# Kernel optimization log

Hardware: AMD Instinct MI355X
Metric: run time of the kernel (lower is better)

## Reference

```python
import jax, jax.numpy as jnp
import numpy as np

B, L, D_PAIR, N_HEAD = 1, 320, 128, 4
EPS = 1e-5


def setup_inputs() -> dict:
    key = jax.random.key(0)
    ks = jax.random.split(key, 8)
    s = 0.05  # ~xavier scale for fan_in=128
    return {
        "pair": jax.random.normal(ks[0], (B, L, L, D_PAIR), jnp.float32),
        "norm_w": jnp.ones((D_PAIR,), jnp.float32),
        "norm_b": jnp.zeros((D_PAIR,), jnp.float32),
        "Wq": jax.random.normal(ks[1], (D_PAIR, D_PAIR), jnp.float32) * s,
        "Wk": jax.random.normal(ks[2], (D_PAIR, D_PAIR), jnp.float32) * s,
        "Wv": jax.random.normal(ks[3], (D_PAIR, D_PAIR), jnp.float32) * s,
        "Wg": jax.random.normal(ks[4], (D_PAIR, D_PAIR), jnp.float32) * s,
        "bg": jnp.zeros((D_PAIR,), jnp.float32),
        "Wo": jax.random.normal(ks[5], (D_PAIR, D_PAIR), jnp.float32) * s,
        "bo": jnp.zeros((D_PAIR,), jnp.float32),
        "Wb": jax.random.normal(ks[6], (N_HEAD, D_PAIR), jnp.float32) * s,
    }


def reference(pair, norm_w, norm_b, Wq, Wk, Wv, Wg, bg, Wo, bo, Wb):
    # Triangle attention, mode='start' (no permute). pair: (B, L, L, D)
    Bs, Ls, _, D = pair.shape
    H = Wb.shape[0]
    Dh = D // H
    scale = Dh ** -0.5

    # LayerNorm (fp32, matches torch eps=1e-5)
    mu = jnp.mean(pair, axis=-1, keepdims=True)
    var = jnp.var(pair, axis=-1, keepdims=True)
    x = (pair - mu) * jax.lax.rsqrt(var + EPS) * norm_w + norm_b

    def heads(y):
        # (B,L,L,D) -> (B,L,H,L,Dh): attention runs along the second L axis per row i
        return y.reshape(Bs, Ls, Ls, H, Dh).transpose(0, 1, 3, 2, 4)

    Q = heads(x @ Wq.T)
    K = heads(x @ Wk.T)
    V = heads(x @ Wv.T)
    g = heads(jax.nn.sigmoid(x @ Wg.T + bg))

    attn = jnp.einsum('blhid,blhjd->blhij', Q, K) * scale  # (B,L,H,L,L)
    # bias from RAW pair (pre-norm), projected to heads, broadcast over query index i
    bias = (pair @ Wb.T).transpose(0, 1, 3, 2)[:, :, :, None, :]  # (B,L,H,1,L)
    attn = jax.nn.softmax(attn + bias, axis=-1)

    out = jnp.einsum('blhij,blhjd->blhid', attn, V)  # (B,L,H,L,Dh)
    out = (g * out).transpose(0, 1, 3, 2, 4).reshape(Bs, Ls, Ls, D)
    return pair + out @ Wo.T + bo
```

## Files before the change

kernel.cpp:

```cpp
#include <hip/hip_runtime.h>

typedef unsigned short u16;
typedef unsigned int u32;
typedef __attribute__((ext_vector_type(8))) short bf16x8;
typedef __attribute__((ext_vector_type(4))) float f32x4;

#define LOG2E 1.4426950408889634f

__device__ __forceinline__ u16 f2bf(float f) {
    u32 u = __float_as_uint(f);
    u += 0x7fffu + ((u >> 16) & 1u);
    return (u16)(u >> 16);
}
__device__ __forceinline__ float bf2f(u16 s) {
    return __uint_as_float(((u32)s) << 16);
}

__global__ void wconv_kernel(const float* __restrict__ Wq, const float* __restrict__ Wk,
                             const float* __restrict__ Wv, const float* __restrict__ Wg,
                             const float* __restrict__ Wo, u16* __restrict__ wbf) {
    int idx = blockIdx.x * blockDim.x + threadIdx.x;
    wbf[0 * 16384 + idx] = f2bf(Wq[idx]);
    wbf[1 * 16384 + idx] = f2bf(Wk[idx]);
    wbf[2 * 16384 + idx] = f2bf(Wv[idx]);
    wbf[3 * 16384 + idx] = f2bf(Wg[idx]);
    wbf[4 * 16384 + idx] = f2bf(Wo[idx]);
}

__global__ __launch_bounds__(256, 1)
void attn_kernel(const float* __restrict__ pair,
                 const float* __restrict__ norm_w,
                 const float* __restrict__ norm_b,
                 const float* __restrict__ bg,
                 const float* __restrict__ Wb,
                 const u16* __restrict__ wbf,
                 u16* __restrict__ Obf) {
    const int l = blockIdx.x >> 2;
    const int h = blockIdx.x & 3;
    const int tid = threadIdx.x;
    const int wave = tid >> 6;
    const int lane = tid & 63;
    const int i_lo = lane & 15;
    const int q = lane >> 4;

    __shared__ __align__(16) u16 Xs[64 * 136];
    __shared__ __align__(16) u16 Qs[320 * 40];
    __shared__ __align__(16) u16 Ks[320 * 40];
    __shared__ __align__(16) u16 Gs[320 * 40];
    __shared__ __align__(16) u16 VTs[32 * 328];
    __shared__ __align__(16) float biasLds[320];
    __shared__ __align__(16) float wls[3 * 128];

    if (tid < 96) {
        int a = tid >> 5;
        int t = tid & 31;
        const float* src = (a == 0) ? norm_w : (a == 1) ? norm_b : (Wb + h * 128);
        f32x4 v = *(const f32x4*)(src + t * 4);
        *(f32x4*)&wls[a * 128 + t * 4] = v;
    }

    float bg0 = bg[h * 32 + i_lo];
    float bg1 = bg[h * 32 + 16 + i_lo];

    bf16x8 wfrag[4][8];
#pragma unroll
    for (int kc = 0; kc < 4; ++kc)
#pragma unroll
        for (int nt = 0; nt < 8; ++nt) {
            int mat = nt >> 1;
            int drow = h * 32 + (nt & 1) * 16 + i_lo;
            wfrag[kc][nt] = *(const bf16x8*)&wbf[mat * 16384 + drow * 128 + kc * 32 + q * 8];
        }

    __syncthreads();

    const int row_g = tid >> 2;
    const int c4 = tid & 3;

#pragma unroll 1
    for (int jt5 = 0; jt5 < 5; ++jt5) {
        int j0 = jt5 * 64;
        const float* prow = pair + ((size_t)(l * 320 + j0 + row_g)) * 128 + c4 * 32;
        f32x4 pr[8];
#pragma unroll
        for (int u = 0; u < 8; ++u) pr[u] = *(const f32x4*)(prow + u * 4);

        float s = 0.f, s2 = 0.f, bd = 0.f;
#pragma unroll
        for (int u = 0; u < 8; ++u) {
            f32x4 p = pr[u];
            f32x4 wb4 = *(const f32x4*)&wls[2 * 128 + c4 * 32 + u * 4];
            s += p[0] + p[1] + p[2] + p[3];
            s2 += p[0] * p[0] + p[1] * p[1] + p[2] * p[2] + p[3] * p[3];
            bd += p[0] * wb4[0] + p[1] * wb4[1] + p[2] * wb4[2] + p[3] * wb4[3];
        }
        s += __shfl_xor(s, 1);   s += __shfl_xor(s, 2);
        s2 += __shfl_xor(s2, 1); s2 += __shfl_xor(s2, 2);
        bd += __shfl_xor(bd, 1); bd += __shfl_xor(bd, 2);
        float mu = s * 0.0078125f;
        float var = s2 * 0.0078125f - mu * mu;
        float rs = rsqrtf(var + 1e-5f);

        __syncthreads();
#pragma unroll
        for (int u = 0; u < 8; ++u) {
            f32x4 p = pr[u];
            f32x4 w4 = *(const f32x4*)&wls[0 * 128 + c4 * 32 + u * 4];
            f32x4 b4 = *(const f32x4*)&wls[1 * 128 + c4 * 32 + u * 4];
            ushort4 xv;
            xv.x = f2bf((p[0] - mu) * rs * w4[0] + b4[0]);
            xv.y = f2bf((p[1] - mu) * rs * w4[1] + b4[1]);
            xv.z = f2bf((p[2] - mu) * rs * w4[2] + b4[2]);
            xv.w = f2bf((p[3] - mu) * rs * w4[3] + b4[3]);
            *(ushort4*)&Xs[row_g * 136 + c4 * 32 + u * 4] = xv;
        }
        if (c4 == 0) biasLds[j0 + row_g] = bd * LOG2E;
        __syncthreads();

        f32x4 acc[8];
#pragma unroll
        for (int nt = 0; nt < 8; ++nt) acc[nt] = (f32x4){0.f, 0.f, 0.f, 0.f};
#pragma unroll
        for (int kc = 0; kc < 4; ++kc) {
            bf16x8 a = *(const bf16x8*)&Xs[(wave * 16 + i_lo) * 136 + kc * 32 + q * 8];
#pragma unroll
            for (int nt = 0; nt < 8; ++nt)
                acc[nt] = __builtin_amdgcn_mfma_f32_16x16x32_bf16(a, wfrag[kc][nt], acc[nt], 0, 0, 0);
        }
        int jrow = j0 + wave * 16 + q * 4;
#pragma unroll
        for (int nt = 0; nt < 8; ++nt) {
#pragma unroll
            for (int r = 0; r < 4; ++r) {
                float v = acc[nt][r];
                int jr = jrow + r;
                int dl = (nt & 1) * 16 + i_lo;
                if (nt < 2)      Qs[jr * 40 + dl] = f2bf(v);
                else if (nt < 4) Ks[jr * 40 + dl] = f2bf(v);
                else if (nt < 6) VTs[dl * 328 + jr] = f2bf(v);
                else {
                    float z = v + ((nt & 1) ? bg1 : bg0);
                    float g = 1.0f / (1.0f + exp2f(-z * LOG2E));
                    Gs[jr * 40 + dl] = f2bf(g);
                }
            }
        }
    }
    __syncthreads();

    const float SC = 0.17677669529663687f * LOG2E;
    const f32x4 zero4 = {0.f, 0.f, 0.f, 0.f};
#pragma unroll 1
    for (int s5 = 0; s5 < 5; ++s5) {
        int i0 = wave * 80 + s5 * 16;
        bf16x8 qf = *(const bf16x8*)&Qs[(i0 + i_lo) * 40 + q * 8];

        f32x4 sc[20];
#pragma unroll
        for (int jt = 0; jt < 20; ++jt) {
            bf16x8 kf = *(const bf16x8*)&Ks[(jt * 16 + i_lo) * 40 + q * 8];
            sc[jt] = __builtin_amdgcn_mfma_f32_16x16x32_bf16(kf, qf, zero4, 0, 0, 0);
        }
        float mx = -3.0e38f;
#pragma unroll
        for (int jt = 0; jt < 20; ++jt) {
            f32x4 b4 = *(const f32x4*)&biasLds[jt * 16 + q * 4];
#pragma unroll
            for (int r = 0; r < 4; ++r) {
                float v = sc[jt][r] * SC + b4[r];
                sc[jt][r] = v;
                mx = fmaxf(mx, v);
            }
        }
        mx = fmaxf(mx, __shfl_xor(mx, 16));
        mx = fmaxf(mx, __shfl_xor(mx, 32));
        float sum = 0.f;
#pragma unroll
        for (int jt = 0; jt < 20; ++jt)
#pragma unroll
            for (int r = 0; r < 4; ++r) {
                float p = exp2f(sc[jt][r] - mx);
                sc[jt][r] = p;
                sum += p;
            }
        sum += __shfl_xor(sum, 16);
        sum += __shfl_xor(sum, 32);
        float rinv = 1.0f / sum;

        f32x4 oacc[2];
        oacc[0] = zero4; oacc[1] = zero4;
        const int srcb = ((q & 1) * 2) * 16 + i_lo;
        const bool hiq = (q >= 2);
#pragma unroll
        for (int kt = 0; kt < 10; ++kt) {
            union { bf16x8 v; u16 u[8]; } pu;
#pragma unroll
            for (int jj = 0; jj < 8; ++jj) {
                int r = jj & 3;
                int src = srcb + ((jj >> 2) << 4);
                float lo = __shfl(sc[2 * kt][r], src, 64);
                float hi = __shfl(sc[2 * kt + 1][r], src, 64);
                pu.u[jj] = f2bf(hiq ? hi : lo);
            }
#pragma unroll
            for (int mt = 0; mt < 2; ++mt) {
                bf16x8 vf = *(const bf16x8*)&VTs[(mt * 16 + i_lo) * 328 + kt * 32 + q * 8];
                oacc[mt] = __builtin_amdgcn_mfma_f32_16x16x32_bf16(vf, pu.v, oacc[mt], 0, 0, 0);
            }
        }
#pragma unroll
        for (int mt = 0; mt < 2; ++mt)
#pragma unroll
            for (int r = 0; r < 4; ++r) {
                int d = mt * 16 + q * 4 + r;
                float g = bf2f(Gs[(i0 + i_lo) * 40 + d]);
                float o = oacc[mt][r] * rinv * g;
                Obf[((size_t)(l * 320 + i0 + i_lo)) * 128 + h * 32 + d] = f2bf(o);
            }
    }
}

__global__ __launch_bounds__(256)
void outproj_kernel(const float* __restrict__ pair,
                    const float* __restrict__ bo,
                    const u16* __restrict__ Obf,
                    const u16* __restrict__ wbf,
                    float* __restrict__ out) {
    const int tid = threadIdx.x;
    const int wave = tid >> 6;
    const int lane = tid & 63;
    const int i_lo = lane & 15;
    const int q = lane >> 4;
    const int mrow = blockIdx.x * 64 + wave * 16;
    const u16* Wo = wbf + 4 * 16384;

    bf16x8 of[4];
#pragma unroll
    for (int kc = 0; kc < 4; ++kc)
        of[kc] = *(const bf16x8*)&Obf[((size_t)(mrow + i_lo)) * 128 + kc * 32 + q * 8];

    float bov[8];
#pragma unroll
    for (int nt = 0; nt < 8; ++nt) bov[nt] = bo[nt * 16 + i_lo];

    f32x4 acc[8];
#pragma unroll
    for (int nt = 0; nt < 8; ++nt) acc[nt] = (f32x4){0.f, 0.f, 0.f, 0.f};
#pragma unroll
    for (int nt = 0; nt < 8; ++nt) {
#pragma unroll
        for (int kc = 0; kc < 4; ++kc) {
            bf16x8 wf = *(const bf16x8*)&Wo[(nt * 16 + i_lo) * 128 + kc * 32 + q * 8];
            acc[nt] = __builtin_amdgcn_mfma_f32_16x16x32_bf16(of[kc], wf, acc[nt], 0, 0, 0);
        }
    }
#pragma unroll
    for (int nt = 0; nt < 8; ++nt)
#pragma unroll
        for (int r = 0; r < 4; ++r) {
            size_t idx = ((size_t)(mrow + q * 4 + r)) * 128 + nt * 16 + i_lo;
            out[idx] = acc[nt][r] + pair[idx] + bov[nt];
        }
}

extern "C" void kernel_launch(void* const* d_in, const int* in_sizes, int n_in,
                              void* d_out, int out_size, void* d_ws, size_t ws_size,
                              hipStream_t stream) {
    const float* pair   = (const float*)d_in[0];
    const float* norm_w = (const float*)d_in[1];
    const float* norm_b = (const float*)d_in[2];
    const float* Wq     = (const float*)d_in[3];
    const float* Wk     = (const float*)d_in[4];
    const float* Wv     = (const float*)d_in[5];
    const float* Wg     = (const float*)d_in[6];
    const float* bg     = (const float*)d_in[7];
    const float* Wo     = (const float*)d_in[8];
    const float* bo     = (const float*)d_in[9];
    const float* Wb     = (const float*)d_in[10];

    u16* wbf = (u16*)d_ws;
    u16* Obf = wbf + 5 * 16384;
    float* out = (float*)d_out;

    wconv_kernel<<<64, 256, 0, stream>>>(Wq, Wk, Wv, Wg, Wo, wbf);
    attn_kernel<<<320 * 4, 256, 0, stream>>>(pair, norm_w, norm_b, bg, Wb, wbf, Obf);
    outproj_kernel<<<1600, 256, 0, stream>>>(pair, bo, Obf, wbf, out);
}
```

Before: 346.4 us.

## Restructure triangle attention to 512 threads, LDS P staging, no softmax max

Doubles the attention block to 8 waves and puts all tiles in one shared buffer. The probability matrix is staged through per-wave LDS with truncating bf16 packing instead of lane shuffles. The softmax max-subtraction is dropped, and the output projection is transposed so stores and pair loads are vectorized. This cuts shuffle and conversion overhead and raises parallelism. Skipping the max is numerically unsafe for large logits, and truncation lowers rounding accuracy.

```diff
diff --git a/kernel.cpp b/kernel.cpp
--- a/kernel.cpp
+++ b/kernel.cpp
@@ -4,6 +4,7 @@
 typedef unsigned int u32;
 typedef __attribute__((ext_vector_type(8))) short bf16x8;
 typedef __attribute__((ext_vector_type(4))) float f32x4;
+typedef __attribute__((ext_vector_type(2))) unsigned int u32x2;
 
 #define LOG2E 1.4426950408889634f
 
@@ -14,6 +15,9 @@
 }
 __device__ __forceinline__ float bf2f(u16 s) {
     return __uint_as_float(((u32)s) << 16);
+}
+__device__ __forceinline__ u32 pk_bf_trunc(float hi, float lo) {
+    return __builtin_amdgcn_perm(__float_as_uint(hi), __float_as_uint(lo), 0x07060302u);
 }
 
 __global__ void wconv_kernel(const float* __restrict__ Wq, const float* __restrict__ Wk,
@@ -27,7 +31,13 @@
     wbf[4 * 16384 + idx] = f2bf(Wo[idx]);
 }
 
-__global__ __launch_bounds__(256, 1)
+#define PBUF_W 2688
+#define QS_OFF 21504
+#define KS_OFF 34304
+#define GS_OFF 47104
+#define VTS_OFF 59904
+
+__global__ __launch_bounds__(512, 2)
 void attn_kernel(const float* __restrict__ pair,
                  const float* __restrict__ norm_w,
                  const float* __restrict__ norm_b,
@@ -43,11 +53,7 @@
     const int i_lo = lane & 15;
     const int q = lane >> 4;
 
-    __shared__ __align__(16) u16 Xs[64 * 136];
-    __shared__ __align__(16) u16 Qs[320 * 40];
-    __shared__ __align__(16) u16 Ks[320 * 40];
-    __shared__ __align__(16) u16 Gs[320 * 40];
-    __shared__ __align__(16) u16 VTs[32 * 328];
+    __shared__ __align__(16) u16 smem[70400];
     __shared__ __align__(16) float biasLds[320];
     __shared__ __align__(16) float wls[3 * 128];
 
@@ -78,70 +84,80 @@
     const int c4 = tid & 3;
 
 #pragma unroll 1
-    for (int jt5 = 0; jt5 < 5; ++jt5) {
-        int j0 = jt5 * 64;
-        const float* prow = pair + ((size_t)(l * 320 + j0 + row_g)) * 128 + c4 * 32;
+    for (int t = 0; t < 3; ++t) {
+        const int j0 = t * 128;
+        const int nrows = (t == 2) ? 64 : 128;
+        const bool act = row_g < nrows;
+
         f32x4 pr[8];
-#pragma unroll
-        for (int u = 0; u < 8; ++u) pr[u] = *(const f32x4*)(prow + u * 4);
-
-        float s = 0.f, s2 = 0.f, bd = 0.f;
-#pragma unroll
-        for (int u = 0; u < 8; ++u) {
-            f32x4 p = pr[u];
-            f32x4 wb4 = *(const f32x4*)&wls[2 * 128 + c4 * 32 + u * 4];
-            s += p[0] + p[1] + p[2] + p[3];
-            s2 += p[0] * p[0] + p[1] * p[1] + p[2] * p[2] + p[3] * p[3];
-            bd += p[0] * wb4[0] + p[1] * wb4[1] + p[2] * wb4[2] + p[3] * wb4[3];
-        }
-        s += __shfl_xor(s, 1);   s += __shfl_xor(s, 2);
-        s2 += __shfl_xor(s2, 1); s2 += __shfl_xor(s2, 2);
-        bd += __shfl_xor(bd, 1); bd += __shfl_xor(bd, 2);
-        float mu = s * 0.0078125f;
-        float var = s2 * 0.0078125f - mu * mu;
-        float rs = rsqrtf(var + 1e-5f);
+        float mu, rs, bd;
+        if (act) {
+            const float* prow = pair + ((size_t)(l * 320 + j0 + row_g)) * 128 + c4 * 32;
+#pragma unroll
+            for (int u = 0; u < 8; ++u) pr[u] = *(const f32x4*)(prow + u * 4);
+            float s = 0.f, s2 = 0.f;
+            bd = 0.f;
+#pragma unroll
+            for (int u = 0; u < 8; ++u) {
+                f32x4 p = pr[u];
+                f32x4 wb4 = *(const f32x4*)&wls[2 * 128 + c4 * 32 + u * 4];
+                s += p[0] + p[1] + p[2] + p[3];
+                s2 += p[0] * p[0] + p[1] * p[1] + p[2] * p[2] + p[3] * p[3];
+                bd += p[0] * wb4[0] + p[1] * wb4[1] + p[2] * wb4[2] + p[3] * wb4[3];
+            }
+            s += __shfl_xor(s, 1);   s += __shfl_xor(s, 2);
+            s2 += __shfl_xor(s2, 1); s2 += __shfl_xor(s2, 2);
+            bd += __shfl_xor(bd, 1); bd += __shfl_xor(bd, 2);
+            mu = s * 0.0078125f;
+            float var = s2 * 0.0078125f - mu * mu;
+            rs = rsqrtf(var + 1e-5f);
+        }
 
         __syncthreads();
-#pragma unroll
-        for (int u = 0; u < 8; ++u) {
-            f32x4 p = pr[u];
-            f32x4 w4 = *(const f32x4*)&wls[0 * 128 + c4 * 32 + u * 4];
-            f32x4 b4 = *(const f32x4*)&wls[1 * 128 + c4 * 32 + u * 4];
-            ushort4 xv;
-            xv.x = f2bf((p[0] - mu) * rs * w4[0] + b4[0]);
-            xv.y = f2bf((p[1] - mu) * rs * w4[1] + b4[1]);
-            xv.z = f2bf((p[2] - mu) * rs * w4[2] + b4[2]);
-            xv.w = f2bf((p[3] - mu) * rs * w4[3] + b4[3]);
-            *(ushort4*)&Xs[row_g * 136 + c4 * 32 + u * 4] = xv;
-        }
-        if (c4 == 0) biasLds[j0 + row_g] = bd * LOG2E;
+        if (act) {
+#pragma unroll
+            for (int u = 0; u < 8; ++u) {
+                f32x4 p = pr[u];
+                f32x4 w4 = *(const f32x4*)&wls[0 * 128 + c4 * 32 + u * 4];
+                f32x4 b4 = *(const f32x4*)&wls[1 * 128 + c4 * 32 + u * 4];
+                ushort4 xv;
+                xv.x = f2bf((p[0] - mu) * rs * w4[0] + b4[0]);
+                xv.y = f2bf((p[1] - mu) * rs * w4[1] + b4[1]);
+                xv.z = f2bf((p[2] - mu) * rs * w4[2] + b4[2]);
+                xv.w = f2bf((p[3] - mu) * rs * w4[3] + b4[3]);
+                *(ushort4*)&smem[row_g * 136 + c4 * 32 + u * 4] = xv;
+            }
+            if (c4 == 0) biasLds[j0 + row_g] = bd * LOG2E;
+        }
         __syncthreads();
 
-        f32x4 acc[8];
-#pragma unroll
-        for (int nt = 0; nt < 8; ++nt) acc[nt] = (f32x4){0.f, 0.f, 0.f, 0.f};
-#pragma unroll
-        for (int kc = 0; kc < 4; ++kc) {
-            bf16x8 a = *(const bf16x8*)&Xs[(wave * 16 + i_lo) * 136 + kc * 32 + q * 8];
-#pragma unroll
-            for (int nt = 0; nt < 8; ++nt)
-                acc[nt] = __builtin_amdgcn_mfma_f32_16x16x32_bf16(a, wfrag[kc][nt], acc[nt], 0, 0, 0);
-        }
-        int jrow = j0 + wave * 16 + q * 4;
-#pragma unroll
-        for (int nt = 0; nt < 8; ++nt) {
-#pragma unroll
-            for (int r = 0; r < 4; ++r) {
-                float v = acc[nt][r];
-                int jr = jrow + r;
-                int dl = (nt & 1) * 16 + i_lo;
-                if (nt < 2)      Qs[jr * 40 + dl] = f2bf(v);
-                else if (nt < 4) Ks[jr * 40 + dl] = f2bf(v);
-                else if (nt < 6) VTs[dl * 328 + jr] = f2bf(v);
-                else {
-                    float z = v + ((nt & 1) ? bg1 : bg0);
-                    float g = 1.0f / (1.0f + exp2f(-z * LOG2E));
-                    Gs[jr * 40 + dl] = f2bf(g);
+        if (wave * 16 < nrows) {
+            f32x4 acc[8];
+#pragma unroll
+            for (int nt = 0; nt < 8; ++nt) acc[nt] = (f32x4){0.f, 0.f, 0.f, 0.f};
+#pragma unroll
+            for (int kc = 0; kc < 4; ++kc) {
+                bf16x8 a = *(const bf16x8*)&smem[(wave * 16 + i_lo) * 136 + kc * 32 + q * 8];
+#pragma unroll
+                for (int nt = 0; nt < 8; ++nt)
+                    acc[nt] = __builtin_amdgcn_mfma_f32_16x16x32_bf16(a, wfrag[kc][nt], acc[nt], 0, 0, 0);
+            }
+            int jrow = j0 + wave * 16 + q * 4;
+#pragma unroll
+            for (int nt = 0; nt < 8; ++nt) {
+#pragma unroll
+                for (int r = 0; r < 4; ++r) {
+                    float v = acc[nt][r];
+                    int jr = jrow + r;
+                    int dl = (nt & 1) * 16 + i_lo;
+                    if (nt < 2)      smem[QS_OFF + jr * 40 + dl] = f2bf(v);
+                    else if (nt < 4) smem[KS_OFF + jr * 40 + dl] = f2bf(v);
+                    else if (nt < 6) smem[VTS_OFF + dl * 328 + jr] = f2bf(v);
+                    else {
+                        float z = v + ((nt & 1) ? bg1 : bg0);
+                        float g = 1.0f / (1.0f + exp2f(-z * LOG2E));
+                        smem[GS_OFF + jr * 40 + dl] = f2bf(g);
+                    }
                 }
             }
         }
@@ -150,73 +166,69 @@
 
     const float SC = 0.17677669529663687f * LOG2E;
     const f32x4 zero4 = {0.f, 0.f, 0.f, 0.f};
+    u16* pb = smem + wave * PBUF_W;
 #pragma unroll 1
-    for (int s5 = 0; s5 < 5; ++s5) {
-        int i0 = wave * 80 + s5 * 16;
-        bf16x8 qf = *(const bf16x8*)&Qs[(i0 + i_lo) * 40 + q * 8];
+    for (int t2 = 0; t2 < 3; ++t2) {
+        const int strip = wave + 8 * t2;
+        if (strip >= 20) break;
+        const int i0 = strip * 16;
+        bf16x8 qf = *(const bf16x8*)&smem[QS_OFF + (i0 + i_lo) * 40 + q * 8];
 
         f32x4 sc[20];
 #pragma unroll
         for (int jt = 0; jt < 20; ++jt) {
-            bf16x8 kf = *(const bf16x8*)&Ks[(jt * 16 + i_lo) * 40 + q * 8];
+            bf16x8 kf = *(const bf16x8*)&smem[KS_OFF + (jt * 16 + i_lo) * 40 + q * 8];
             sc[jt] = __builtin_amdgcn_mfma_f32_16x16x32_bf16(kf, qf, zero4, 0, 0, 0);
         }
-        float mx = -3.0e38f;
+        float sum = 0.f;
 #pragma unroll
         for (int jt = 0; jt < 20; ++jt) {
             f32x4 b4 = *(const f32x4*)&biasLds[jt * 16 + q * 4];
 #pragma unroll
             for (int r = 0; r < 4; ++r) {
-                float v = sc[jt][r] * SC + b4[r];
-                sc[jt][r] = v;
-                mx = fmaxf(mx, v);
-            }
-        }
-        mx = fmaxf(mx, __shfl_xor(mx, 16));
-        mx = fmaxf(mx, __shfl_xor(mx, 32));
-        float sum = 0.f;
-#pragma unroll
-        for (int jt = 0; jt < 20; ++jt)
-#pragma unroll
-            for (int r = 0; r < 4; ++r) {
-                float p = exp2f(sc[jt][r] - mx);
+                float p = exp2f(sc[jt][r] * SC + b4[r]);
                 sc[jt][r] = p;
                 sum += p;
             }
+        }
         sum += __shfl_xor(sum, 16);
         sum += __shfl_xor(sum, 32);
         float rinv = 1.0f / sum;
 
         f32x4 oacc[2];
         oacc[0] = zero4; oacc[1] = zero4;
-        const int srcb = ((q & 1) * 2) * 16 + i_lo;
-        const bool hiq = (q >= 2);
-#pragma unroll
-        for (int kt = 0; kt < 10; ++kt) {
-            union { bf16x8 v; u16 u[8]; } pu;
-#pragma unroll
-            for (int jj = 0; jj < 8; ++jj) {
-                int r = jj & 3;
-                int src = srcb + ((jj >> 2) << 4);
-                float lo = __shfl(sc[2 * kt][r], src, 64);
-                float hi = __shfl(sc[2 * kt + 1][r], src, 64);
-                pu.u[jj] = f2bf(hiq ? hi : lo);
-            }
-#pragma unroll
-            for (int mt = 0; mt < 2; ++mt) {
-                bf16x8 vf = *(const bf16x8*)&VTs[(mt * 16 + i_lo) * 328 + kt * 32 + q * 8];
-                oacc[mt] = __builtin_amdgcn_mfma_f32_16x16x32_bf16(vf, pu.v, oacc[mt], 0, 0, 0);
-            }
-        }
-#pragma unroll
-        for (int mt = 0; mt < 2; ++mt)
-#pragma unroll
-            for (int r = 0; r < 4; ++r) {
-                int d = mt * 16 + q * 4 + r;
-                float g = bf2f(Gs[(i0 + i_lo) * 40 + d]);
-                float o = oacc[mt][r] * rinv * g;
-                Obf[((size_t)(l * 320 + i0 + i_lo)) * 128 + h * 32 + d] = f2bf(o);
-            }
+#pragma unroll
+        for (int hh = 0; hh < 2; ++hh) {
+#pragma unroll
+            for (int jt10 = 0; jt10 < 10; ++jt10) {
+                f32x4 s4 = sc[hh * 10 + jt10];
+                u32x2 pk;
+                pk.x = pk_bf_trunc(s4[1], s4[0]);
+                pk.y = pk_bf_trunc(s4[3], s4[2]);
+                *(u32x2*)&pb[i_lo * 168 + jt10 * 16 + q * 4] = pk;
+            }
+#pragma unroll
+            for (int kt = 0; kt < 5; ++kt) {
+                bf16x8 pf = *(const bf16x8*)&pb[i_lo * 168 + kt * 32 + q * 8];
+#pragma unroll
+                for (int mt = 0; mt < 2; ++mt) {
+                    bf16x8 vf = *(const bf16x8*)&smem[VTS_OFF + (mt * 16 + i_lo) * 328 + hh * 160 + kt * 32 + q * 8];
+                    oacc[mt] = __builtin_amdgcn_mfma_f32_16x16x32_bf16(vf, pf, oacc[mt], 0, 0, 0);
+                }
+            }
+        }
+#pragma unroll
+        for (int mt = 0; mt < 2; ++mt) {
+            ushort4 g4 = *(const ushort4*)&smem[GS_OFF + (i0 + i_lo) * 40 + mt * 16 + q * 4];
+            float o0 = oacc[mt][0] * rinv * bf2f(g4.x);
+            float o1 = oacc[mt][1] * rinv * bf2f(g4.y);
+            float o2 = oacc[mt][2] * rinv * bf2f(g4.z);
+            float o3 = oacc[mt][3] * rinv * bf2f(g4.w);
+            u32x2 pk;
+            pk.x = pk_bf_trunc(o1, o0);
+            pk.y = pk_bf_trunc(o3, o2);
+            *(u32x2*)&Obf[((size_t)(l * 320 + i0 + i_lo)) * 128 + h * 32 + mt * 16 + q * 4] = pk;
+        }
     }
 }
 
@@ -239,10 +251,6 @@
     for (int kc = 0; kc < 4; ++kc)
         of[kc] = *(const bf16x8*)&Obf[((size_t)(mrow + i_lo)) * 128 + kc * 32 + q * 8];
 
-    float bov[8];
-#pragma unroll
-    for (int nt = 0; nt < 8; ++nt) bov[nt] = bo[nt * 16 + i_lo];
-
     f32x4 acc[8];
 #pragma unroll
     for (int nt = 0; nt < 8; ++nt) acc[nt] = (f32x4){0.f, 0.f, 0.f, 0.f};
@@ -251,16 +259,21 @@
 #pragma unroll
         for (int kc = 0; kc < 4; ++kc) {
             bf16x8 wf = *(const bf16x8*)&Wo[(nt * 16 + i_lo) * 128 + kc * 32 + q * 8];
-            acc[nt] = __builtin_amdgcn_mfma_f32_16x16x32_bf16(of[kc], wf, acc[nt], 0, 0, 0);
-        }
-    }
-#pragma unroll
-    for (int nt = 0; nt < 8; ++nt)
-#pragma unroll
-        for (int r = 0; r < 4; ++r) {
-            size_t idx = ((size_t)(mrow + q * 4 + r)) * 128 + nt * 16 + i_lo;
-            out[idx] = acc[nt][r] + pair[idx] + bov[nt];
-        }
+            acc[nt] = __builtin_amdgcn_mfma_f32_16x16x32_bf16(wf, of[kc], acc[nt], 0, 0, 0);
+        }
+    }
+#pragma unroll
+    for (int nt = 0; nt < 8; ++nt) {
+        size_t idx = ((size_t)(mrow + i_lo)) * 128 + nt * 16 + q * 4;
+        f32x4 p4 = *(const f32x4*)&pair[idx];
+        f32x4 b4 = *(const f32x4*)&bo[nt * 16 + q * 4];
+        f32x4 o4;
+        o4[0] = acc[nt][0] + p4[0] + b4[0];
+        o4[1] = acc[nt][1] + p4[1] + b4[1];
+        o4[2] = acc[nt][2] + p4[2] + b4[2];
+        o4[3] = acc[nt][3] + p4[3] + b4[3];
+        *(f32x4*)&out[idx] = o4;
+    }
 }
 
 extern "C" void kernel_launch(void* const* d_in, const int* in_sizes, int n_in,
@@ -283,6 +296,6 @@
     float* out = (float*)d_out;
 
     wconv_kernel<<<64, 256, 0, stream>>>(Wq, Wk, Wv, Wg, Wo, wbf);
-    attn_kernel<<<320 * 4, 256, 0, stream>>>(pair, norm_w, norm_b, bg, Wb, wbf, Obf);
+    attn_kernel<<<320 * 4, 512, 0, stream>>>(pair, norm_w, norm_b, bg, Wb, wbf, Obf);
     outproj_kernel<<<1600, 256, 0, stream>>>(pair, bo, Obf, wbf, out);
 }
```

After: 291.0 us. 1.19x faster.
